# Optimization experiments

Measured on AMD Instinct MI355X. Metric: run time of the kernel, lower is better.

Reference implementation:

```python
import jax, jax.numpy as jnp
import numpy as np

# ---- module config (matches init_kwargs) ----
OGFH, OGFW = 256, 704
DOWNSAMPLE = 8
FH, FW = OGFH // DOWNSAMPLE, OGFW // DOWNSAMPLE   # 32, 88
DBOUND = (4.0, 45.0, 1.0)
D = int((DBOUND[1] - DBOUND[0]) / DBOUND[2])      # 41 depth bins
CAMC = 64
XB = (-50.0, 50.0, 0.5)    # lateral  -> nx = 200
YB = (-10.0, 10.0, 20.0)   # vertical -> ny = 1
ZB = (0.0, 50.0, 0.25)     # depth    -> nz = 200
NX = np.array([int((b[1] - b[0]) / b[2]) for b in (XB, YB, ZB)])  # [200, 1, 200]
DX = np.array([b[2] for b in (XB, YB, ZB)], dtype=np.float32)
BX = np.array([b[0] + b[2] / 2.0 for b in (XB, YB, ZB)], dtype=np.float32)


def make_frustum():
    # matches create_frustum_1camera: [D, fH, fW, 3] of (u, v, depth)
    ds = jnp.broadcast_to(
        jnp.arange(DBOUND[0], DBOUND[1], DBOUND[2], dtype=jnp.float32)[:, None, None],
        (D, FH, FW))
    xs = jnp.broadcast_to(
        jnp.linspace(0.0, OGFW - 1, FW, dtype=jnp.float32)[None, None, :], (D, FH, FW))
    ys = jnp.broadcast_to(
        jnp.linspace(0.0, OGFH - 1, FH, dtype=jnp.float32)[None, :, None], (D, FH, FW))
    return jnp.stack((xs, ys, ds), -1)


def setup_inputs() -> dict:
    key = jax.random.key(0)
    B = 4
    # depthnet output: first D channels = depth logits, next CAMC = context feats
    x = jax.random.normal(key, (B, D + CAMC, FH, FW), dtype=jnp.float32)
    fx = fy = 520.0
    K = jnp.array([[fx, 0.0, OGFW / 2.0],
                   [0.0, fy, OGFH / 2.0],
                   [0.0, 0.0, 1.0]], dtype=jnp.float32)
    intrins = jnp.broadcast_to(K, (B, 3, 3))
    post_rots = jnp.broadcast_to(jnp.eye(3, dtype=jnp.float32), (B, 3, 3))
    post_trans = jnp.zeros((B, 3), dtype=jnp.float32)
    return {"x": x, "intrins": intrins, "post_rots": post_rots, "post_trans": post_trans}


def _forward(x, intrins, post_rots, post_trans):
    B = x.shape[0]
    frustum = make_frustum()                                                     # [D,H,W,3]
    # ---- get_geometry ----
    pts = frustum[None] - post_trans[:, None, None, None, :]                     # [B,D,H,W,3]
    pts = jnp.einsum('bij,bdhwj->bdhwi', jnp.linalg.inv(post_rots), pts)
    pts = jnp.concatenate([pts[..., :2] * pts[..., 2:3], pts[..., 2:3]], -1)     # un-normalize
    geom = jnp.einsum('bij,bdhwj->bdhwi', jnp.linalg.inv(intrins), pts)          # [B,D,H,W,3]
    # ---- lift: depth softmax (x) context features ----
    depth = jax.nn.softmax(x[:, :D], axis=1)                                     # [B,D,H,W]
    feat = x[:, D:D + CAMC]                                                      # [B,C,H,W]
    vol = depth[:, None] * feat[:, :, None]                                      # [B,C,D,H,W]
    vol = jnp.transpose(vol, (0, 2, 3, 4, 1))                                    # [B,D,H,W,C]
    # ---- voxel_splat (sort+cumsum trick == segmented sum) ----
    Nprime = B * D * FH * FW
    feats = vol.reshape(Nprime, CAMC)
    # torch .long() truncates toward zero -> astype(int32)
    coords = ((geom - (BX - DX / 2.0)) / DX).astype(jnp.int32).reshape(Nprime, 3)
    bix = jnp.repeat(jnp.arange(B, dtype=jnp.int32), Nprime // B)
    kept = ((coords[:, 0] >= 0) & (coords[:, 0] < int(NX[0])) &
            (coords[:, 1] >= 0) & (coords[:, 1] < int(NX[1])) &
            (coords[:, 2] >= 0) & (coords[:, 2] < int(NX[2])))
    nseg = int(NX[0] * NX[1] * NX[2]) * B
    ranks = (coords[:, 0] * (int(NX[1]) * int(NX[2]) * B)
             + coords[:, 1] * (int(NX[2]) * B)
             + coords[:, 2] * B + bix)
    ranks = jnp.where(kept, ranks, nseg)  # dump bucket for dropped points
    pooled = jax.ops.segment_sum(jnp.where(kept[:, None], feats, 0.0), ranks,
                                 num_segments=nseg + 1)[:nseg]
    final = pooled.reshape(int(NX[0]), int(NX[1]), int(NX[2]), B, CAMC)          # [x,y,z,B,C]
    final = jnp.transpose(final, (3, 4, 1, 2, 0))                                # [B,C,ny,nz,nx]
    # torch.cat(final.unbind(dim=2), 1): collapse ny into channels (y-major)
    final = jnp.transpose(final, (0, 2, 1, 3, 4)).reshape(
        B, CAMC * int(NX[1]), int(NX[2]), int(NX[0]))                            # [B,C,200,200]
    return final


def reference(x, intrins, post_rots, post_trans):
    return _forward(x, intrins, post_rots, post_trans)
```

## Files before the change

### kernel.cpp

```cpp
#include <hip/hip_runtime.h>
#include <math.h>

#define DD   41
#define FHh  32
#define FWw  88
#define CC   64
#define CH   32
#define CG8  8
#define NXx  200
#define NZz  200
#define NCH  (DD + CC)
#define PLANE ((size_t)FHh * FWw)
#define NE   (DD * FWw)
#define DCAP 4
#define OVCAP 4096

__global__ __launch_bounds__(256) void lss_colpool(
    const float* __restrict__ x,
    const float* __restrict__ intrins,
    const float* __restrict__ post_rots,
    const float* __restrict__ post_trans,
    float* __restrict__ P, int* __restrict__ V,
    int* __restrict__ rowcnt8, int* __restrict__ ovcnt,
    float* __restrict__ out, int out_quads)
{
    __shared__ float Wt[DD][FHh + 1];
    __shared__ float F4s[FHh][36];
    __shared__ float Mi[18];
    __shared__ float pm[8][FHh + 1];
    __shared__ int   Vtmp[DD];

    int blk   = blockIdx.x;
    int chalf = blk & 1;
    int w     = (blk >> 1) % FWw;
    int b     = blk / (2 * FWw);
    int t     = threadIdx.x;
    const float* xb = x + (size_t)b * NCH * PLANE + w;

    for (int idx = t; idx < DD * FHh; idx += 256) {
        int d = idx >> 5, h = idx & 31;
        Wt[d][h] = xb[((size_t)d * FHh + h) * FWw];
    }
    for (int idx = t; idx < FHh * CH; idx += 256) {
        int c = idx & 31, h = idx >> 5;
        F4s[h][c] = xb[((size_t)(DD + chalf * CH + c) * FHh + h) * FWw];
    }
    if (t >= 64 && t < 64 + DD) Vtmp[t - 64] = -1;
    if (t == 0) {
        #pragma clang fp contract(off)
        for (int m = 0; m < 2; ++m) {
            const float* A = (m == 0 ? post_rots : intrins) + b * 9;
            float* O = Mi + m * 9;
            float a = A[0], bb = A[1], c = A[2];
            float d = A[3], e  = A[4], f = A[5];
            float g = A[6], h  = A[7], i = A[8];
            float det = a * (e * i - f * h) - bb * (d * i - f * g) + c * (d * h - e * g);
            O[0] = (e * i - f * h) / det;
            O[1] = (c * h - bb * i) / det;
            O[2] = (bb * f - c * e) / det;
            O[3] = (f * g - d * i) / det;
            O[4] = (a * i - c * g) / det;
            O[5] = (c * d - a * f) / det;
            O[6] = (d * h - e * g) / det;
            O[7] = (bb * g - a * h) / det;
            O[8] = (a * e - bb * d) / det;
        }
    }
    __syncthreads();

    int h = t & 31, l = t >> 5;
    float e_[6];
    {
        float pmax = -INFINITY;
        for (int d = l; d < DD; d += 8) pmax = fmaxf(pmax, Wt[d][h]);
        pm[l][h] = pmax;
    }
    __syncthreads();
    float mx = -INFINITY;
    for (int j = 0; j < 8; ++j) mx = fmaxf(mx, pm[j][h]);
    __syncthreads();
    {
        #pragma clang fp contract(off)
        float psum = 0.0f;
        int k = 0;
        for (int d = l; d < DD; d += 8, ++k) {
            float e = expf(Wt[d][h] - mx);
            e_[k] = e; psum += e;
        }
        pm[l][h] = psum;
    }
    __syncthreads();
    float s = 0.0f;
    for (int j = 0; j < 8; ++j) s += pm[j][h];

    {
        #pragma clang fp contract(off)
        float xs = (float)((double)w * 703.0 / 87.0);
        float ys = (float)((double)h * 255.0 / 31.0);
        float tx = post_trans[b * 3 + 0];
        float ty = post_trans[b * 3 + 1];
        float tz = post_trans[b * 3 + 2];
        int k = 0;
        for (int d = l; d < DD; d += 8, ++k) {
            float z  = 4.0f + (float)d;
            float px = xs - tx, py = ys - ty, pz = z - tz;
            float rx = Mi[0] * px + Mi[1] * py + Mi[2] * pz;
            float ry = Mi[3] * px + Mi[4] * py + Mi[5] * pz;
            float rz = Mi[6] * px + Mi[7] * py + Mi[8] * pz;
            float qx = rx * rz, qy = ry * rz, qz = rz;
            float gx = Mi[ 9] * qx + Mi[10] * qy + Mi[11] * qz;
            float gy = Mi[12] * qx + Mi[13] * qy + Mi[14] * qz;
            float gz = Mi[15] * qx + Mi[16] * qy + Mi[17] * qz;
            float cx = (gx + 50.0f) / 0.5f;
            float cy = (gy + 10.0f) / 20.0f;
            float cz = gz / 0.25f;
            int ix = (int)cx;
            int iy = (int)cy;
            int iz = (int)cz;
            bool kept = (ix >= 0) & (ix < NXx) & (iy == 0) & (iz >= 0) & (iz < NZz);
            if (kept) {
                Wt[d][h] = e_[k] / s;
                Vtmp[d] = iz * NXx + ix;
            } else {
                Wt[d][h] = 0.0f;
            }
        }
    }
    __syncthreads();

    float* Pb = P + ((size_t)b * NE) * CC + chalf * CH;
    {
        int c4 = t & 7;
        for (int d = t >> 3; d < DD; d += 32) {
            float4 acc = make_float4(0.f, 0.f, 0.f, 0.f);
            for (int hh = 0; hh < FHh; ++hh) {
                float wtv = Wt[d][hh];
                float4 fv = *(const float4*)&F4s[hh][c4 * 4];
                acc.x += wtv * fv.x; acc.y += wtv * fv.y;
                acc.z += wtv * fv.z; acc.w += wtv * fv.w;
            }
            *(float4*)&Pb[((size_t)d * FWw + w) * CC + c4 * 4] = acc;
        }
    }
    if (chalf == 0) {
        if (t < DD) V[(size_t)b * NE + (size_t)t * FWw + w] = Vtmp[t];
        if (w == 0) for (int i = t; i < NZz * 8; i += 256) rowcnt8[b * NZz * 8 + i] = 0;
    }
    if (blk == 0 && t == 0) *ovcnt = 0;

    {
        float4 z = make_float4(0.f, 0.f, 0.f, 0.f);
        float4* o4 = (float4*)out;
        int stride = gridDim.x * 256;
        for (int i = blk * 256 + t; i < out_quads; i += stride) o4[i] = z;
    }
}

__global__ __launch_bounds__(256) void lss_rowbuild(
    const float* __restrict__ P, const int* __restrict__ V,
    float* __restrict__ S, int* __restrict__ izd,
    int* __restrict__ rowcnt8, int* __restrict__ dlist8,
    int* __restrict__ ovcnt, int* __restrict__ ovlist,
    float* __restrict__ out)
{
    __shared__ float acc[CG8 * (NXx + 1)];
    __shared__ int ixw[FWw];
    __shared__ int izw[FWw];
    __shared__ int key;
    __shared__ int s_k;

    int blk = blockIdx.x;
    int cg = blk & 7;
    int bd = blk >> 3;
    int d = bd % DD;
    int b = bd / DD;
    int t = threadIdx.x;

    if (t == 0) key = 0x7fffffff;
    for (int i = t; i < CG8 * (NXx + 1); i += 256) acc[i] = 0.0f;
    __syncthreads();
    if (t < FWw) {
        int v = V[(size_t)bd * FWw + t];
        if (v >= 0) {
            int iz = v / NXx;
            izw[t] = iz; ixw[t] = v - iz * NXx;
            atomicMin(&key, (t << 16) | iz);
        } else { izw[t] = -1; ixw[t] = -1; }
    }
    __syncthreads();
    int kk = key;
    int s_iz = (kk == 0x7fffffff) ? -1 : (kk & 0xffff);
    if (cg == 0 && t == 0) izd[bd] = s_iz;
    if (s_iz < 0) return;

    int r = b * NZz + s_iz;
    if (t == 0) {
        int k = atomicAdd(&rowcnt8[r * 8 + cg], 1);
        if (k < DCAP) dlist8[(r * 8 + cg) * DCAP + k] = d;
        s_k = k;
    }
    if (cg == 0 && t < FWw && izw[t] >= 0 && izw[t] != s_iz) {
        int k = atomicAdd(ovcnt, 1);
        if (k < OVCAP)
            ovlist[k] = (b << 29) | (d << 23) | (t << 16) | (ixw[t] << 8) | izw[t];
    }

    const float* Pb = P + (size_t)bd * FWw * CC + cg * CG8;
    for (int idx = t; idx < FWw * 2; idx += 256) {
        int w = idx >> 1, q = idx & 1;
        if (izw[w] == s_iz) {
            float4 v = *(const float4*)&Pb[(size_t)w * CC + q * 4];
            int ix = ixw[w];
            int cb = q * 4;
            atomicAdd(&acc[(cb + 0) * (NXx + 1) + ix], v.x);
            atomicAdd(&acc[(cb + 1) * (NXx + 1) + ix], v.y);
            atomicAdd(&acc[(cb + 2) * (NXx + 1) + ix], v.z);
            atomicAdd(&acc[(cb + 3) * (NXx + 1) + ix], v.w);
        }
    }
    __syncthreads();

    bool owner0 = (s_k == 0);
    for (int i = t; i < CG8 * (NXx / 4); i += 256) {
        int c = i / (NXx / 4), q = i - c * (NXx / 4);
        int base = c * (NXx + 1) + q * 4;
        float4 vv;
        vv.x = acc[base + 0];
        vv.y = acc[base + 1];
        vv.z = acc[base + 2];
        vv.w = acc[base + 3];
        if (owner0) {
            float* orow = out + (((size_t)(b * CC + cg * CG8 + c)) * NZz + s_iz) * NXx;
            ((float4*)orow)[q] = vv;
        } else {
            float* Srow = S + ((size_t)bd * CC + cg * CG8 + c) * NXx;
            ((float4*)Srow)[q] = vv;
        }
    }
}

__global__ __launch_bounds__(256) void lss_fixup(
    const float* __restrict__ S, const int* __restrict__ izd,
    const int* __restrict__ rowcnt8, const int* __restrict__ dlist8,
    const float* __restrict__ P,
    const int* __restrict__ ovcnt, const int* __restrict__ ovlist,
    float* __restrict__ out)
{
    int b = blockIdx.x;
    int t = threadIdx.x;

    for (int pair = t; pair < NZz * 8; pair += 256) {
        int n = rowcnt8[b * NZz * 8 + pair];
        if (n <= 1) continue;
        int iz = pair >> 3, cg = pair & 7;
        const int* dl = dlist8 + (size_t)(b * NZz * 8 + pair) * DCAP;
        if (n <= DCAP) {
            for (int k = 1; k < n; ++k) {
                int d = dl[k];
                for (int c = 0; c < CG8; ++c) {
                    const float* Srow = S + ((size_t)(b * DD + d) * CC + cg * CG8 + c) * NXx;
                    float* orow = out + (((size_t)(b * CC + cg * CG8 + c)) * NZz + iz) * NXx;
                    for (int ix = 0; ix < NXx; ++ix) atomicAdd(&orow[ix], Srow[ix]);
                }
            }
        } else {
            int owner0 = dl[0];
            for (int d = 0; d < DD; ++d) {
                if (izd[b * DD + d] == iz && d != owner0) {
                    for (int c = 0; c < CG8; ++c) {
                        const float* Srow = S + ((size_t)(b * DD + d) * CC + cg * CG8 + c) * NXx;
                        float* orow = out + (((size_t)(b * CC + cg * CG8 + c)) * NZz + iz) * NXx;
                        for (int ix = 0; ix < NXx; ++ix) atomicAdd(&orow[ix], Srow[ix]);
                    }
                }
            }
        }
    }

    if (b == 0 && t == 0) {
        int nov = *ovcnt;
        if (nov > OVCAP) nov = OVCAP;
        for (int k = 0; k < nov; ++k) {
            int ent = ovlist[k];
            int eb  = (ent >> 29) & 7;
            int ed  = (ent >> 23) & 63;
            int ew  = (ent >> 16) & 127;
            int eix = (ent >> 8) & 255;
            int eiz = ent & 255;
            for (int c = 0; c < CC; ++c) {
                size_t o = (((size_t)(eb * CC + c)) * NZz + eiz) * NXx + eix;
                atomicAdd(&out[o], P[(((size_t)eb * DD + ed) * FWw + ew) * CC + c]);
            }
        }
    }
}

extern "C" void kernel_launch(void* const* d_in, const int* in_sizes, int n_in,
                              void* d_out, int out_size, void* d_ws, size_t ws_size,
                              hipStream_t stream)
{
    const float* x          = (const float*)d_in[0];
    const float* intrins    = (const float*)d_in[1];
    const float* post_rots  = (const float*)d_in[2];
    const float* post_trans = (const float*)d_in[3];
    float* out = (float*)d_out;

    int B = in_sizes[0] / (NCH * (int)PLANE);

    size_t off = 0;
    auto alloc = [&](size_t bytes) {
        void* p = (char*)d_ws + off;
        off = (off + bytes + 255) & ~(size_t)255;
        return p;
    };
    float* P       = (float*)alloc((size_t)B * NE * CC * sizeof(float));
    int*   V       = (int*)  alloc((size_t)B * NE * sizeof(int));
    float* S       = (float*)alloc((size_t)B * DD * CC * NXx * sizeof(float));
    int*   izd     = (int*)  alloc((size_t)B * DD * sizeof(int));
    int*   rowcnt8 = (int*)  alloc((size_t)B * NZz * 8 * sizeof(int));
    int*   dlist8  = (int*)  alloc((size_t)B * NZz * 8 * DCAP * sizeof(int));
    int*   ovcnt   = (int*)  alloc(256);
    int*   ovlist  = (int*)  alloc((size_t)OVCAP * sizeof(int));

    int out_quads = out_size / 4;

    lss_colpool<<<B * FWw * 2, 256, 0, stream>>>(x, intrins, post_rots, post_trans,
                                                 P, V, rowcnt8, ovcnt, out, out_quads);
    lss_rowbuild<<<B * DD * 8, 256, 0, stream>>>(P, V, S, izd, rowcnt8, dlist8,
                                                 ovcnt, ovlist, out);
    lss_fixup<<<B, 256, 0, stream>>>(S, izd, rowcnt8, dlist8, P, ovcnt, ovlist, out);
}
```

Before: 100.2 us.

## Scatter column-pooled features directly into output with global atomics

Drops the intermediate P/V buffers and the row-build and fixup kernels. The column-pooling kernel now atomically adds each depth bin's pooled 64-channel vector straight into the BEV output, and skips bins that fall outside the grid. Output zeroing moves into its own small kernel that runs before the fused one. This removes two kernel launches, the workspace traffic and the serial single-thread overflow pass, at the cost of many scattered global float atomics and a summation order that is no longer deterministic.

```diff
diff --git a/kernel.cpp b/kernel.cpp
--- a/kernel.cpp
+++ b/kernel.cpp
@@ -6,23 +6,25 @@
 #define FWw  88
 #define CC   64
 #define CH   32
-#define CG8  8
 #define NXx  200
 #define NZz  200
 #define NCH  (DD + CC)
 #define PLANE ((size_t)FHh * FWw)
-#define NE   (DD * FWw)
-#define DCAP 4
-#define OVCAP 4096
+#define VOXB (NZz * NXx)
 
-__global__ __launch_bounds__(256) void lss_colpool(
+__global__ __launch_bounds__(256) void lss_zero(float4* __restrict__ o4, int nq)
+{
+    float4 z = make_float4(0.f, 0.f, 0.f, 0.f);
+    int stride = gridDim.x * 256;
+    for (int i = blockIdx.x * 256 + threadIdx.x; i < nq; i += stride) o4[i] = z;
+}
+
+__global__ __launch_bounds__(256) void lss_fused(
     const float* __restrict__ x,
     const float* __restrict__ intrins,
     const float* __restrict__ post_rots,
     const float* __restrict__ post_trans,
-    float* __restrict__ P, int* __restrict__ V,
-    int* __restrict__ rowcnt8, int* __restrict__ ovcnt,
-    float* __restrict__ out, int out_quads)
+    float* __restrict__ out)
 {
     __shared__ float Wt[DD][FHh + 1];
     __shared__ float F4s[FHh][36];
@@ -128,10 +130,12 @@
     }
     __syncthreads();
 
-    float* Pb = P + ((size_t)b * NE) * CC + chalf * CH;
+    float* ob = out + ((size_t)b * CC + chalf * CH) * VOXB;
     {
         int c4 = t & 7;
         for (int d = t >> 3; d < DD; d += 32) {
+            int v = Vtmp[d];
+            if (v < 0) continue;
             float4 acc = make_float4(0.f, 0.f, 0.f, 0.f);
             for (int hh = 0; hh < FHh; ++hh) {
                 float wtv = Wt[d][hh];
@@ -139,158 +143,11 @@
                 acc.x += wtv * fv.x; acc.y += wtv * fv.y;
                 acc.z += wtv * fv.z; acc.w += wtv * fv.w;
             }
-            *(float4*)&Pb[((size_t)d * FWw + w) * CC + c4 * 4] = acc;
-        }
-    }
-    if (chalf == 0) {
-        if (t < DD) V[(size_t)b * NE + (size_t)t * FWw + w] = Vtmp[t];
-        if (w == 0) for (int i = t; i < NZz * 8; i += 256) rowcnt8[b * NZz * 8 + i] = 0;
-    }
-    if (blk == 0 && t == 0) *ovcnt = 0;
-
-    {
-        float4 z = make_float4(0.f, 0.f, 0.f, 0.f);
-        float4* o4 = (float4*)out;
-        int stride = gridDim.x * 256;
-        for (int i = blk * 256 + t; i < out_quads; i += stride) o4[i] = z;
-    }
-}
-
-__global__ __launch_bounds__(256) void lss_rowbuild(
-    const float* __restrict__ P, const int* __restrict__ V,
-    float* __restrict__ S, int* __restrict__ izd,
-    int* __restrict__ rowcnt8, int* __restrict__ dlist8,
-    int* __restrict__ ovcnt, int* __restrict__ ovlist,
-    float* __restrict__ out)
-{
-    __shared__ float acc[CG8 * (NXx + 1)];
-    __shared__ int ixw[FWw];
-    __shared__ int izw[FWw];
-    __shared__ int key;
-    __shared__ int s_k;
-
-    int blk = blockIdx.x;
-    int cg = blk & 7;
-    int bd = blk >> 3;
-    int d = bd % DD;
-    int b = bd / DD;
-    int t = threadIdx.x;
-
-    if (t == 0) key = 0x7fffffff;
-    for (int i = t; i < CG8 * (NXx + 1); i += 256) acc[i] = 0.0f;
-    __syncthreads();
-    if (t < FWw) {
-        int v = V[(size_t)bd * FWw + t];
-        if (v >= 0) {
-            int iz = v / NXx;
-            izw[t] = iz; ixw[t] = v - iz * NXx;
-            atomicMin(&key, (t << 16) | iz);
-        } else { izw[t] = -1; ixw[t] = -1; }
-    }
-    __syncthreads();
-    int kk = key;
-    int s_iz = (kk == 0x7fffffff) ? -1 : (kk & 0xffff);
-    if (cg == 0 && t == 0) izd[bd] = s_iz;
-    if (s_iz < 0) return;
-
-    int r = b * NZz + s_iz;
-    if (t == 0) {
-        int k = atomicAdd(&rowcnt8[r * 8 + cg], 1);
-        if (k < DCAP) dlist8[(r * 8 + cg) * DCAP + k] = d;
-        s_k = k;
-    }
-    if (cg == 0 && t < FWw && izw[t] >= 0 && izw[t] != s_iz) {
-        int k = atomicAdd(ovcnt, 1);
-        if (k < OVCAP)
-            ovlist[k] = (b << 29) | (d << 23) | (t << 16) | (ixw[t] << 8) | izw[t];
-    }
-
-    const float* Pb = P + (size_t)bd * FWw * CC + cg * CG8;
-    for (int idx = t; idx < FWw * 2; idx += 256) {
-        int w = idx >> 1, q = idx & 1;
-        if (izw[w] == s_iz) {
-            float4 v = *(const float4*)&Pb[(size_t)w * CC + q * 4];
-            int ix = ixw[w];
-            int cb = q * 4;
-            atomicAdd(&acc[(cb + 0) * (NXx + 1) + ix], v.x);
-            atomicAdd(&acc[(cb + 1) * (NXx + 1) + ix], v.y);
-            atomicAdd(&acc[(cb + 2) * (NXx + 1) + ix], v.z);
-            atomicAdd(&acc[(cb + 3) * (NXx + 1) + ix], v.w);
-        }
-    }
-    __syncthreads();
-
-    bool owner0 = (s_k == 0);
-    for (int i = t; i < CG8 * (NXx / 4); i += 256) {
-        int c = i / (NXx / 4), q = i - c * (NXx / 4);
-        int base = c * (NXx + 1) + q * 4;
-        float4 vv;
-        vv.x = acc[base + 0];
-        vv.y = acc[base + 1];
-        vv.z = acc[base + 2];
-        vv.w = acc[base + 3];
-        if (owner0) {
-            float* orow = out + (((size_t)(b * CC + cg * CG8 + c)) * NZz + s_iz) * NXx;
-            ((float4*)orow)[q] = vv;
-        } else {
-            float* Srow = S + ((size_t)bd * CC + cg * CG8 + c) * NXx;
-            ((float4*)Srow)[q] = vv;
-        }
-    }
-}
-
-__global__ __launch_bounds__(256) void lss_fixup(
-    const float* __restrict__ S, const int* __restrict__ izd,
-    const int* __restrict__ rowcnt8, const int* __restrict__ dlist8,
-    const float* __restrict__ P,
-    const int* __restrict__ ovcnt, const int* __restrict__ ovlist,
-    float* __restrict__ out)
-{
-    int b = blockIdx.x;
-    int t = threadIdx.x;
-
-    for (int pair = t; pair < NZz * 8; pair += 256) {
-        int n = rowcnt8[b * NZz * 8 + pair];
-        if (n <= 1) continue;
-        int iz = pair >> 3, cg = pair & 7;
-        const int* dl = dlist8 + (size_t)(b * NZz * 8 + pair) * DCAP;
-        if (n <= DCAP) {
-            for (int k = 1; k < n; ++k) {
-                int d = dl[k];
-                for (int c = 0; c < CG8; ++c) {
-                    const float* Srow = S + ((size_t)(b * DD + d) * CC + cg * CG8 + c) * NXx;
-                    float* orow = out + (((size_t)(b * CC + cg * CG8 + c)) * NZz + iz) * NXx;
-                    for (int ix = 0; ix < NXx; ++ix) atomicAdd(&orow[ix], Srow[ix]);
-                }
-            }
-        } else {
-            int owner0 = dl[0];
-            for (int d = 0; d < DD; ++d) {
-                if (izd[b * DD + d] == iz && d != owner0) {
-                    for (int c = 0; c < CG8; ++c) {
-                        const float* Srow = S + ((size_t)(b * DD + d) * CC + cg * CG8 + c) * NXx;
-                        float* orow = out + (((size_t)(b * CC + cg * CG8 + c)) * NZz + iz) * NXx;
-                        for (int ix = 0; ix < NXx; ++ix) atomicAdd(&orow[ix], Srow[ix]);
-                    }
-                }
-            }
-        }
-    }
-
-    if (b == 0 && t == 0) {
-        int nov = *ovcnt;
-        if (nov > OVCAP) nov = OVCAP;
-        for (int k = 0; k < nov; ++k) {
-            int ent = ovlist[k];
-            int eb  = (ent >> 29) & 7;
-            int ed  = (ent >> 23) & 63;
-            int ew  = (ent >> 16) & 127;
-            int eix = (ent >> 8) & 255;
-            int eiz = ent & 255;
-            for (int c = 0; c < CC; ++c) {
-                size_t o = (((size_t)(eb * CC + c)) * NZz + eiz) * NXx + eix;
-                atomicAdd(&out[o], P[(((size_t)eb * DD + ed) * FWw + ew) * CC + c]);
-            }
+            float* p0 = ob + (size_t)(c4 * 4) * VOXB + v;
+            atomicAdd(p0,             acc.x);
+            atomicAdd(p0 + VOXB,      acc.y);
+            atomicAdd(p0 + 2 * VOXB,  acc.z);
+            atomicAdd(p0 + 3 * VOXB,  acc.w);
         }
     }
 }
@@ -307,26 +164,10 @@
 
     int B = in_sizes[0] / (NCH * (int)PLANE);
 
-    size_t off = 0;
-    auto alloc = [&](size_t bytes) {
-        void* p = (char*)d_ws + off;
-        off = (off + bytes + 255) & ~(size_t)255;
-        return p;
-    };
-    float* P       = (float*)alloc((size_t)B * NE * CC * sizeof(float));
-    int*   V       = (int*)  alloc((size_t)B * NE * sizeof(int));
-    float* S       = (float*)alloc((size_t)B * DD * CC * NXx * sizeof(float));
-    int*   izd     = (int*)  alloc((size_t)B * DD * sizeof(int));
-    int*   rowcnt8 = (int*)  alloc((size_t)B * NZz * 8 * sizeof(int));
-    int*   dlist8  = (int*)  alloc((size_t)B * NZz * 8 * DCAP * sizeof(int));
-    int*   ovcnt   = (int*)  alloc(256);
-    int*   ovlist  = (int*)  alloc((size_t)OVCAP * sizeof(int));
+    int out_quads = out_size / 4;
+    int zb = (out_quads + 255) / 256;
+    if (zb > 2048) zb = 2048;
 
-    int out_quads = out_size / 4;
-
-    lss_colpool<<<B * FWw * 2, 256, 0, stream>>>(x, intrins, post_rots, post_trans,
-                                                 P, V, rowcnt8, ovcnt, out, out_quads);
-    lss_rowbuild<<<B * DD * 8, 256, 0, stream>>>(P, V, S, izd, rowcnt8, dlist8,
-                                                 ovcnt, ovlist, out);
-    lss_fixup<<<B, 256, 0, stream>>>(S, izd, rowcnt8, dlist8, P, ovcnt, ovlist, out);
+    lss_zero <<<zb, 256, 0, stream>>>((float4*)out, out_quads);
+    lss_fused<<<B * FWw * 2, 256, 0, stream>>>(x, intrins, post_rots, post_trans, out);
 }
```

Result: slower. 145.4 us (+45.1%).
